# Performance work log

Measured on AMD Instinct MI355X. Metric: run time of the kernel, lower is better.

## Reference

```python
import jax, jax.numpy as jnp
import numpy as np

B, T, S, H = 4, 256, 512, 512


def setup_inputs() -> dict:
    key = jax.random.key(0)
    ks = jax.random.split(key, 8)
    scale = 1.0 / np.sqrt(H)
    return {
        "decoder_hidden": jax.random.normal(ks[0], (B, T, H), jnp.float32),
        "encoder_outputs": jax.random.normal(ks[1], (B, S, H), jnp.float32),
        "W1": jax.random.uniform(ks[2], (H, H), jnp.float32, -scale, scale),
        "b1": jax.random.uniform(ks[3], (H,), jnp.float32, -scale, scale),
        "W2": jax.random.uniform(ks[4], (H, H), jnp.float32, -scale, scale),
        "b2": jax.random.uniform(ks[5], (H,), jnp.float32, -scale, scale),
        "V": jax.random.uniform(ks[6], (H,), jnp.float32, -scale, scale),
        "bV": jax.random.uniform(ks[7], (), jnp.float32, -scale, scale),
    }


def reference(decoder_hidden, encoder_outputs, W1, b1, W2, b2, V, bV):
    # Projections: q (B,T,H), k (B,S,H)
    q = jnp.einsum("bth,hd->btd", decoder_hidden, W1.T) + b1
    k = jnp.einsum("bsh,hd->bsd", encoder_outputs, W2.T) + b2
    # Additive scores: tanh over broadcast (B,T,S,H), reduced by V -> (B,T,S)
    e = jnp.tanh(q[:, :, None, :] + k[:, None, :, :])
    score = jnp.einsum("btsh,h->bts", e, V) + bV
    attn = jax.nn.softmax(score, axis=-1)
    # Context: (B,T,S) @ (B,S,H) -> (B,T,H)
    context = jnp.einsum("bts,bsh->bth", attn, encoder_outputs)
    return context
```

## Files before the change

### kernel.cpp

```cpp
#include <hip/hip_runtime.h>

#define B 4
#define T 256
#define S 512
#define H 512
#define BT (B*T)
#define PCTX_STRIDE ((size_t)BT * H)

#define PRESCALE 2.8853900817779268f
#define LOG2E 1.4426950408889634f
#define QCLAMP 15.0f

typedef unsigned short u16;
typedef __attribute__((ext_vector_type(8))) short bf16x8;
typedef __attribute__((ext_vector_type(4))) float f32x4;

#if __has_builtin(__builtin_amdgcn_exp2f)
#define EXP2(x) __builtin_amdgcn_exp2f(x)
#else
#define EXP2(x) exp2f(x)
#endif

__device__ __forceinline__ u16 f2bf(float x) {
    unsigned u = __float_as_uint(x);
    u = u + 0x7FFFu + ((u >> 16) & 1u);
    return (u16)(u >> 16);
}

__device__ __forceinline__ void split8(float4 f0, float4 f1, bf16x8& hi, bf16x8& lo) {
    float x[8] = {f0.x, f0.y, f0.z, f0.w, f1.x, f1.y, f1.z, f1.w};
    #pragma unroll
    for (int i = 0; i < 8; ++i) {
        unsigned u = __float_as_uint(x[i]);
        unsigned h = u & 0xFFFF0000u;
        hi[i] = (short)(h >> 16);
        lo[i] = (short)f2bf(x[i] - __uint_as_float(h));
    }
}

__global__ __launch_bounds__(256) void mfma_proj(
    const float* __restrict__ dh, const float* __restrict__ enc,
    const float* __restrict__ W1, const float* __restrict__ W2,
    const float* __restrict__ b1, const float* __restrict__ b2,
    float* __restrict__ abuf, float* __restrict__ bT4)
{
    __shared__ u16 lds[4 * 4096];

    const int tid   = threadIdx.x;
    const int lane  = tid & 63;
    const int w     = tid >> 6;
    const int n0    = blockIdx.x * 64;
    const int mTile = blockIdx.y;
    const int mbase = mTile * 64;
    const bool is_q = (mTile < 16);

    const float* Asrc = is_q ? dh : enc;
    const float* Wsrc = is_q ? W1 : W2;
    const int arow = is_q ? mbase : (mbase - 1024);

    const int wm = (w & 1) * 32;
    const int wn = (w >> 1) * 32;

    const int r0  = tid >> 3;
    const int kc0 = tid & 7;

    f32x4 acc[2][2] = {};

    for (int kb = 0; kb < 8; ++kb) {
        const int k0 = kb * 64 + kc0 * 8;
        const size_t ga0 = (size_t)(arow + r0) * 512 + k0;
        const size_t ga1 = (size_t)(arow + r0 + 32) * 512 + k0;
        const size_t gw0 = (size_t)(n0 + r0) * 512 + k0;
        const size_t gw1 = (size_t)(n0 + r0 + 32) * 512 + k0;
        bf16x8 ah0, al0, ah1, al1, wh0, wl0, wh1, wl1;
        split8(*(const float4*)&Asrc[ga0], *(const float4*)&Asrc[ga0 + 4], ah0, al0);
        split8(*(const float4*)&Asrc[ga1], *(const float4*)&Asrc[ga1 + 4], ah1, al1);
        split8(*(const float4*)&Wsrc[gw0], *(const float4*)&Wsrc[gw0 + 4], wh0, wl0);
        split8(*(const float4*)&Wsrc[gw1], *(const float4*)&Wsrc[gw1 + 4], wh1, wl1);
        __syncthreads();
        const int sw  = (kc0 ^ (r0 & 7)) << 3;
        const int s0o = r0 * 64 + sw;
        const int s1o = (r0 + 32) * 64 + sw;
        *(bf16x8*)&lds[0 * 4096 + s0o] = ah0;  *(bf16x8*)&lds[0 * 4096 + s1o] = ah1;
        *(bf16x8*)&lds[1 * 4096 + s0o] = al0;  *(bf16x8*)&lds[1 * 4096 + s1o] = al1;
        *(bf16x8*)&lds[2 * 4096 + s0o] = wh0;  *(bf16x8*)&lds[2 * 4096 + s1o] = wh1;
        *(bf16x8*)&lds[3 * 4096 + s0o] = wl0;  *(bf16x8*)&lds[3 * 4096 + s1o] = wl1;
        __syncthreads();

        #pragma unroll
        for (int ks = 0; ks < 2; ++ks) {
            const int kg = ks * 4 + (lane >> 4);
            bf16x8 amh[2], aml[2], bnh[2], bnl[2];
            #pragma unroll
            for (int ms = 0; ms < 2; ++ms) {
                const int row = wm + ms * 16 + (lane & 15);
                const int off = row * 64 + ((kg ^ (row & 7)) << 3);
                amh[ms] = *(const bf16x8*)&lds[0 * 4096 + off];
                aml[ms] = *(const bf16x8*)&lds[1 * 4096 + off];
            }
            #pragma unroll
            for (int ns = 0; ns < 2; ++ns) {
                const int row = wn + ns * 16 + (lane & 15);
                const int off = row * 64 + ((kg ^ (row & 7)) << 3);
                bnh[ns] = *(const bf16x8*)&lds[2 * 4096 + off];
                bnl[ns] = *(const bf16x8*)&lds[3 * 4096 + off];
            }
            #pragma unroll
            for (int ms = 0; ms < 2; ++ms)
                #pragma unroll
                for (int ns = 0; ns < 2; ++ns) {
                    acc[ms][ns] = __builtin_amdgcn_mfma_f32_16x16x32_bf16(amh[ms], bnh[ns], acc[ms][ns], 0, 0, 0);
                    acc[ms][ns] = __builtin_amdgcn_mfma_f32_16x16x32_bf16(amh[ms], bnl[ns], acc[ms][ns], 0, 0, 0);
                    acc[ms][ns] = __builtin_amdgcn_mfma_f32_16x16x32_bf16(aml[ms], bnh[ns], acc[ms][ns], 0, 0, 0);
                }
        }
    }

    const float* bias = is_q ? b1 : b2;
    #pragma unroll
    for (int ns = 0; ns < 2; ++ns) {
        const int gn = n0 + wn + ns * 16 + (lane & 15);
        const float bv = bias[gn];
        #pragma unroll
        for (int ms = 0; ms < 2; ++ms) {
            #pragma unroll
            for (int r = 0; r < 4; ++r) {
                const int gm = mbase + wm + ms * 16 + (lane >> 4) * 4 + r;
                const float e = EXP2(fminf((acc[ms][ns][r] + bv) * PRESCALE, QCLAMP));
                if (is_q) {
                    abuf[(size_t)gm * 512 + gn] = e;
                } else {
                    const int srow = gm - 1024;
                    const int bb = srow >> 9, ss = srow & 511;
                    bT4[(((size_t)(bb * 128 + (gn >> 2)) * 512) + ss) * 4 + (gn & 3)] = e;
                }
            }
        }
    }
}

__device__ __forceinline__ float quad_term(float4 qa, float4 kb, float4 v4, float acc) {
    float x0 = fmaf(qa.x, kb.x, 1.f);
    float x1 = fmaf(qa.y, kb.y, 1.f);
    float x2 = fmaf(qa.z, kb.z, 1.f);
    float x3 = fmaf(qa.w, kb.w, 1.f);
    float p01 = x0 * x1, p23 = x2 * x3;
    float n01 = fmaf(v4.y, x0, v4.x * x1);
    float n23 = fmaf(v4.w, x2, v4.z * x3);
    float num = fmaf(n23, p01, n01 * p23);
    float den = p01 * p23;
    return fmaf(num, __builtin_amdgcn_rcpf(den), acc);
}

__global__ __launch_bounds__(256) void score_ctx(
    const float* __restrict__ abuf, const float* __restrict__ bT4,
    const float* __restrict__ enc,
    const float* __restrict__ Vp, const float* __restrict__ bVp,
    float* __restrict__ pctx, float* __restrict__ pmz)
{
    __shared__ float e_lds[8][64];

    const int tid  = threadIdx.x;
    const int lane = tid & 63;
    const int w    = tid >> 6;
    const int sc   = blockIdx.x;
    const int t0   = blockIdx.y * 8;
    const int b    = blockIdx.z;
    const int s0   = sc * 64;

    float pv = 0.f;
    #pragma unroll
    for (int i = 0; i < 8; ++i) pv += Vp[i * 64 + lane];
    #pragma unroll
    for (int off = 32; off; off >>= 1) pv += __shfl_xor(pv, off);
    pv += bVp[0];

    const int ta = t0 + w * 2;
    const int tb = ta + 1;
    const float* aA = abuf + __builtin_amdgcn_readfirstlane((b * T + ta) * H);
    const float* aB = abuf + __builtin_amdgcn_readfirstlane((b * T + tb) * H);
    const float4* bp = (const float4*)bT4 + (size_t)(b * 128) * S + s0 + lane;

    float accA = 0.f, accB = 0.f;
    #pragma unroll 4
    for (int h4 = 0; h4 < 128; ++h4) {
        float4 kb = bp[(size_t)h4 * S];
        float4 v4 = *(const float4*)&Vp[h4 * 4];
        float4 qA = *(const float4*)&aA[h4 * 4];
        float4 qB = *(const float4*)&aB[h4 * 4];
        accA = quad_term(qA, kb, v4, accA);
        accB = quad_term(qB, kb, v4, accB);
    }
    const float xA = fmaf(-2.f, accA, pv);
    const float xB = fmaf(-2.f, accB, pv);

    float mA = xA, mB = xB;
    #pragma unroll
    for (int off = 32; off; off >>= 1) {
        mA = fmaxf(mA, __shfl_xor(mA, off));
        mB = fmaxf(mB, __shfl_xor(mB, off));
    }
    const float eA = EXP2((xA - mA) * LOG2E);
    const float eB = EXP2((xB - mB) * LOG2E);
    float zA = eA, zB = eB;
    #pragma unroll
    for (int off = 32; off; off >>= 1) {
        zA += __shfl_xor(zA, off);
        zB += __shfl_xor(zB, off);
    }

    e_lds[w * 2][lane]     = eA;
    e_lds[w * 2 + 1][lane] = eB;
    if (lane == 0) {
        const size_t rowA = (size_t)sc * BT + b * T + ta;
        const size_t rowB = rowA + 1;
        pmz[rowA * 2]     = mA;  pmz[rowA * 2 + 1] = zA;
        pmz[rowB * 2]     = mB;  pmz[rowB * 2 + 1] = zB;
    }
    __syncthreads();

    const float* encb = enc + ((size_t)(b * S + s0)) * H + lane * 8;
    float4 c0A = {0,0,0,0}, c1A = {0,0,0,0}, c0B = {0,0,0,0}, c1B = {0,0,0,0};
    const float* erowA = &e_lds[w * 2][0];
    const float* erowB = &e_lds[w * 2 + 1][0];
    #pragma unroll 4
    for (int si = 0; si < 64; ++si) {
        float4 e0 = *(const float4*)&encb[(size_t)si * H];
        float4 e1 = *(const float4*)&encb[(size_t)si * H + 4];
        const float ea = erowA[si];
        const float eb = erowB[si];
        c0A.x = fmaf(ea, e0.x, c0A.x); c0A.y = fmaf(ea, e0.y, c0A.y);
        c0A.z = fmaf(ea, e0.z, c0A.z); c0A.w = fmaf(ea, e0.w, c0A.w);
        c1A.x = fmaf(ea, e1.x, c1A.x); c1A.y = fmaf(ea, e1.y, c1A.y);
        c1A.z = fmaf(ea, e1.z, c1A.z); c1A.w = fmaf(ea, e1.w, c1A.w);
        c0B.x = fmaf(eb, e0.x, c0B.x); c0B.y = fmaf(eb, e0.y, c0B.y);
        c0B.z = fmaf(eb, e0.z, c0B.z); c0B.w = fmaf(eb, e0.w, c0B.w);
        c1B.x = fmaf(eb, e1.x, c1B.x); c1B.y = fmaf(eb, e1.y, c1B.y);
        c1B.z = fmaf(eb, e1.z, c1B.z); c1B.w = fmaf(eb, e1.w, c1B.w);
    }

    float* outA = pctx + ((size_t)sc * BT + b * T + ta) * H + lane * 8;
    float* outB = pctx + ((size_t)sc * BT + b * T + tb) * H + lane * 8;
    *(float4*)outA = c0A; *(float4*)(outA + 4) = c1A;
    *(float4*)outB = c0B; *(float4*)(outB + 4) = c1B;
}

__global__ __launch_bounds__(256) void combine(
    const float* __restrict__ pctx, const float* __restrict__ pmz,
    float* __restrict__ out)
{
    const int tid  = threadIdx.x;
    const int lane = tid & 63;
    const int row  = blockIdx.x * 4 + (tid >> 6);
    const size_t urow = (size_t)__builtin_amdgcn_readfirstlane(row);

    float m[8], z[8];
    #pragma unroll
    for (int c = 0; c < 8; ++c) {
        m[c] = pmz[((size_t)c * BT + urow) * 2];
        z[c] = pmz[((size_t)c * BT + urow) * 2 + 1];
    }
    float M = m[0];
    #pragma unroll
    for (int c = 1; c < 8; ++c) M = fmaxf(M, m[c]);
    float s[8]; float Z = 0.f;
    #pragma unroll
    for (int c = 0; c < 8; ++c) { s[c] = EXP2((m[c] - M) * LOG2E); Z = fmaf(s[c], z[c], Z); }
    const float inv = __builtin_amdgcn_rcpf(Z);

    #pragma unroll
    for (int j = 0; j < 2; ++j) {
        const size_t f4 = urow * 128 + lane + j * 64;
        float4 acc = {0,0,0,0};
        #pragma unroll
        for (int c = 0; c < 8; ++c) {
            float4 p = ((const float4*)pctx)[(size_t)c * (PCTX_STRIDE / 4) + f4];
            acc.x = fmaf(s[c], p.x, acc.x);
            acc.y = fmaf(s[c], p.y, acc.y);
            acc.z = fmaf(s[c], p.z, acc.z);
            acc.w = fmaf(s[c], p.w, acc.w);
        }
        acc.x *= inv; acc.y *= inv; acc.z *= inv; acc.w *= inv;
        ((float4*)out)[f4] = acc;
    }
}

extern "C" void kernel_launch(void* const* d_in, const int* in_sizes, int n_in,
                              void* d_out, int out_size, void* d_ws, size_t ws_size,
                              hipStream_t stream) {
    const float* dh  = (const float*)d_in[0];
    const float* enc = (const float*)d_in[1];
    const float* W1  = (const float*)d_in[2];
    const float* b1  = (const float*)d_in[3];
    const float* W2  = (const float*)d_in[4];
    const float* b2  = (const float*)d_in[5];
    const float* V   = (const float*)d_in[6];
    const float* bV  = (const float*)d_in[7];

    float* abuf = (float*)d_ws;
    float* bT4  = abuf + (size_t)B * T * H;
    float* pctx = bT4 + (size_t)B * S * H;
    float* pmz  = pctx + 8 * PCTX_STRIDE;

    dim3 blk(256);
    mfma_proj<<<dim3(8, 48),    blk, 0, stream>>>(dh, enc, W1, W2, b1, b2, abuf, bT4);
    score_ctx<<<dim3(8, 32, 4), blk, 0, stream>>>(abuf, bT4, enc, V, bV, pctx, pmz);
    combine  <<<dim3(256),      blk, 0, stream>>>(pctx, pmz, (float*)d_out);
}
```

Baseline: 68.54 us.

## Compute context with split-bf16 MFMA GEMM instead of FMA partials and combine

Replaces the per-chunk FP32 FMA context accumulation and separate combine kernel with an MFMA GEMM over unnormalized exp scores, using hi/lo bf16 splitting for near-fp32 accuracy. The projection kernel gains extra blocks that transpose and split the encoder outputs into bf16 hi/lo. The softmax max subtraction is dropped, relying on the tanh-bounded score range, so only partial sums Z are written. This removes the large partial-context buffer traffic but adds transposed copies and an extra GEMM kernel with a small grid (128 blocks).

```diff
diff --git a/kernel.cpp b/kernel.cpp
--- a/kernel.cpp
+++ b/kernel.cpp
@@ -5,7 +5,6 @@
 #define S 512
 #define H 512
 #define BT (B*T)
-#define PCTX_STRIDE ((size_t)BT * H)
 
 #define PRESCALE 2.8853900817779268f
 #define LOG2E 1.4426950408889634f
@@ -42,15 +41,55 @@
     const float* __restrict__ dh, const float* __restrict__ enc,
     const float* __restrict__ W1, const float* __restrict__ W2,
     const float* __restrict__ b1, const float* __restrict__ b2,
-    float* __restrict__ abuf, float* __restrict__ bT4)
+    float* __restrict__ abuf, float* __restrict__ bT4,
+    u16* __restrict__ encT_hi, u16* __restrict__ encT_lo)
 {
     __shared__ u16 lds[4 * 4096];
 
     const int tid   = threadIdx.x;
+    const int n0    = blockIdx.x * 64;
+    const int mTile = blockIdx.y;
+
+    if (mTile >= 48) {
+        float (*TTf)[65] = reinterpret_cast<float(*)[65]>(lds);
+        const int ty = mTile - 48;
+        const int bb = ty >> 3;
+        const int st = ty & 7;
+        const int c64 = tid & 63;
+        const int r4  = tid >> 6;
+        #pragma unroll
+        for (int rr = 0; rr < 16; ++rr) {
+            const int r = rr * 4 + r4;
+            TTf[r][c64] = enc[((size_t)(bb * S + st * 64 + r)) * H + n0 + c64];
+        }
+        __syncthreads();
+        const int hr = tid >> 2;
+        const int sq = (tid & 3) * 16;
+        u16* ehp = encT_hi + ((size_t)(bb * H + n0 + hr)) * S + st * 64 + sq;
+        u16* elp = encT_lo + ((size_t)(bb * H + n0 + hr)) * S + st * 64 + sq;
+        #pragma unroll
+        for (int j4 = 0; j4 < 4; ++j4) {
+            ushort4 hv, lv;
+            #pragma unroll
+            for (int jj = 0; jj < 4; ++jj) {
+                float x = TTf[sq + j4 * 4 + jj][hr];
+                unsigned u = __float_as_uint(x);
+                unsigned hb = u & 0xFFFF0000u;
+                u16 hh = (u16)(hb >> 16);
+                u16 ll = f2bf(x - __uint_as_float(hb));
+                if (jj == 0) { hv.x = hh; lv.x = ll; }
+                else if (jj == 1) { hv.y = hh; lv.y = ll; }
+                else if (jj == 2) { hv.z = hh; lv.z = ll; }
+                else { hv.w = hh; lv.w = ll; }
+            }
+            *(ushort4*)&ehp[j4 * 4] = hv;
+            *(ushort4*)&elp[j4 * 4] = lv;
+        }
+        return;
+    }
+
     const int lane  = tid & 63;
     const int w     = tid >> 6;
-    const int n0    = blockIdx.x * 64;
-    const int mTile = blockIdx.y;
     const int mbase = mTile * 64;
     const bool is_q = (mTile < 16);
 
@@ -152,14 +191,11 @@
     return fmaf(num, __builtin_amdgcn_rcpf(den), acc);
 }
 
-__global__ __launch_bounds__(256) void score_ctx(
+__global__ __launch_bounds__(256) void score_e(
     const float* __restrict__ abuf, const float* __restrict__ bT4,
-    const float* __restrict__ enc,
     const float* __restrict__ Vp, const float* __restrict__ bVp,
-    float* __restrict__ pctx, float* __restrict__ pmz)
+    u16* __restrict__ e_hi, u16* __restrict__ e_lo, float* __restrict__ Zp)
 {
-    __shared__ float e_lds[8][64];
-
     const int tid  = threadIdx.x;
     const int lane = tid & 63;
     const int w    = tid >> 6;
@@ -194,14 +230,9 @@
     const float xA = fmaf(-2.f, accA, pv);
     const float xB = fmaf(-2.f, accB, pv);
 
-    float mA = xA, mB = xB;
-    #pragma unroll
-    for (int off = 32; off; off >>= 1) {
-        mA = fmaxf(mA, __shfl_xor(mA, off));
-        mB = fmaxf(mB, __shfl_xor(mB, off));
-    }
-    const float eA = EXP2((xA - mA) * LOG2E);
-    const float eB = EXP2((xB - mB) * LOG2E);
+    const float eA = EXP2(xA * LOG2E);
+    const float eB = EXP2(xB * LOG2E);
+
     float zA = eA, zB = eB;
     #pragma unroll
     for (int off = 32; off; off >>= 1) {
@@ -209,79 +240,117 @@
         zB += __shfl_xor(zB, off);
     }
 
-    e_lds[w * 2][lane]     = eA;
-    e_lds[w * 2 + 1][lane] = eB;
+    unsigned uA = __float_as_uint(eA), uB = __float_as_uint(eB);
+    unsigned hA = uA & 0xFFFF0000u,   hB = uB & 0xFFFF0000u;
+    const size_t rowA = (size_t)(b * T + ta);
+    const size_t rowB = (size_t)(b * T + tb);
+    e_hi[rowA * S + s0 + lane] = (u16)(hA >> 16);
+    e_lo[rowA * S + s0 + lane] = f2bf(eA - __uint_as_float(hA));
+    e_hi[rowB * S + s0 + lane] = (u16)(hB >> 16);
+    e_lo[rowB * S + s0 + lane] = f2bf(eB - __uint_as_float(hB));
+
     if (lane == 0) {
-        const size_t rowA = (size_t)sc * BT + b * T + ta;
-        const size_t rowB = rowA + 1;
-        pmz[rowA * 2]     = mA;  pmz[rowA * 2 + 1] = zA;
-        pmz[rowB * 2]     = mB;  pmz[rowB * 2 + 1] = zB;
-    }
-    __syncthreads();
-
-    const float* encb = enc + ((size_t)(b * S + s0)) * H + lane * 8;
-    float4 c0A = {0,0,0,0}, c1A = {0,0,0,0}, c0B = {0,0,0,0}, c1B = {0,0,0,0};
-    const float* erowA = &e_lds[w * 2][0];
-    const float* erowB = &e_lds[w * 2 + 1][0];
-    #pragma unroll 4
-    for (int si = 0; si < 64; ++si) {
-        float4 e0 = *(const float4*)&encb[(size_t)si * H];
-        float4 e1 = *(const float4*)&encb[(size_t)si * H + 4];
-        const float ea = erowA[si];
-        const float eb = erowB[si];
-        c0A.x = fmaf(ea, e0.x, c0A.x); c0A.y = fmaf(ea, e0.y, c0A.y);
-        c0A.z = fmaf(ea, e0.z, c0A.z); c0A.w = fmaf(ea, e0.w, c0A.w);
-        c1A.x = fmaf(ea, e1.x, c1A.x); c1A.y = fmaf(ea, e1.y, c1A.y);
-        c1A.z = fmaf(ea, e1.z, c1A.z); c1A.w = fmaf(ea, e1.w, c1A.w);
-        c0B.x = fmaf(eb, e0.x, c0B.x); c0B.y = fmaf(eb, e0.y, c0B.y);
-        c0B.z = fmaf(eb, e0.z, c0B.z); c0B.w = fmaf(eb, e0.w, c0B.w);
-        c1B.x = fmaf(eb, e1.x, c1B.x); c1B.y = fmaf(eb, e1.y, c1B.y);
-        c1B.z = fmaf(eb, e1.z, c1B.z); c1B.w = fmaf(eb, e1.w, c1B.w);
-    }
-
-    float* outA = pctx + ((size_t)sc * BT + b * T + ta) * H + lane * 8;
-    float* outB = pctx + ((size_t)sc * BT + b * T + tb) * H + lane * 8;
-    *(float4*)outA = c0A; *(float4*)(outA + 4) = c1A;
-    *(float4*)outB = c0B; *(float4*)(outB + 4) = c1B;
-}
-
-__global__ __launch_bounds__(256) void combine(
-    const float* __restrict__ pctx, const float* __restrict__ pmz,
-    float* __restrict__ out)
+        Zp[(size_t)sc * BT + rowA] = zA;
+        Zp[(size_t)sc * BT + rowB] = zB;
+    }
+}
+
+__global__ __launch_bounds__(256) void ctx_mfma(
+    const u16* __restrict__ e_hi, const u16* __restrict__ e_lo,
+    const u16* __restrict__ eT_hi, const u16* __restrict__ eT_lo,
+    const float* __restrict__ Zp, float* __restrict__ out)
 {
+    __shared__ u16 lds[4 * 4096];
+    __shared__ float zinv[64];
+
     const int tid  = threadIdx.x;
     const int lane = tid & 63;
-    const int row  = blockIdx.x * 4 + (tid >> 6);
-    const size_t urow = (size_t)__builtin_amdgcn_readfirstlane(row);
-
-    float m[8], z[8];
-    #pragma unroll
-    for (int c = 0; c < 8; ++c) {
-        m[c] = pmz[((size_t)c * BT + urow) * 2];
-        z[c] = pmz[((size_t)c * BT + urow) * 2 + 1];
-    }
-    float M = m[0];
-    #pragma unroll
-    for (int c = 1; c < 8; ++c) M = fmaxf(M, m[c]);
-    float s[8]; float Z = 0.f;
-    #pragma unroll
-    for (int c = 0; c < 8; ++c) { s[c] = EXP2((m[c] - M) * LOG2E); Z = fmaf(s[c], z[c], Z); }
-    const float inv = __builtin_amdgcn_rcpf(Z);
-
-    #pragma unroll
-    for (int j = 0; j < 2; ++j) {
-        const size_t f4 = urow * 128 + lane + j * 64;
-        float4 acc = {0,0,0,0};
-        #pragma unroll
-        for (int c = 0; c < 8; ++c) {
-            float4 p = ((const float4*)pctx)[(size_t)c * (PCTX_STRIDE / 4) + f4];
-            acc.x = fmaf(s[c], p.x, acc.x);
-            acc.y = fmaf(s[c], p.y, acc.y);
-            acc.z = fmaf(s[c], p.z, acc.z);
-            acc.w = fmaf(s[c], p.w, acc.w);
-        }
-        acc.x *= inv; acc.y *= inv; acc.z *= inv; acc.w *= inv;
-        ((float4*)out)[f4] = acc;
+    const int w    = tid >> 6;
+    const int n0   = blockIdx.x * 64;
+    const int m0   = blockIdx.y * 64;
+    const int b    = blockIdx.z;
+
+    if (tid < 64) {
+        float z = 0.f;
+        #pragma unroll
+        for (int c = 0; c < 8; ++c) z += Zp[(size_t)c * BT + b * T + m0 + tid];
+        zinv[tid] = __builtin_amdgcn_rcpf(z);
+    }
+
+    const int wm = (w & 1) * 32;
+    const int wn = (w >> 1) * 32;
+    const int r0  = tid >> 3;
+    const int kc0 = tid & 7;
+
+    const size_t abase = (size_t)(b * T + m0);
+    const size_t bbase = (size_t)b * H + n0;
+
+    f32x4 acc[2][2] = {};
+
+    for (int kb = 0; kb < 8; ++kb) {
+        const int k0 = kb * 64 + kc0 * 8;
+        const size_t ga0 = (abase + r0) * S + k0;
+        const size_t ga1 = (abase + r0 + 32) * S + k0;
+        const size_t gw0 = (bbase + r0) * S + k0;
+        const size_t gw1 = (bbase + r0 + 32) * S + k0;
+        bf16x8 ah0 = *(const bf16x8*)&e_hi[ga0];
+        bf16x8 ah1 = *(const bf16x8*)&e_hi[ga1];
+        bf16x8 al0 = *(const bf16x8*)&e_lo[ga0];
+        bf16x8 al1 = *(const bf16x8*)&e_lo[ga1];
+        bf16x8 wh0 = *(const bf16x8*)&eT_hi[gw0];
+        bf16x8 wh1 = *(const bf16x8*)&eT_hi[gw1];
+        bf16x8 wl0 = *(const bf16x8*)&eT_lo[gw0];
+        bf16x8 wl1 = *(const bf16x8*)&eT_lo[gw1];
+        __syncthreads();
+        const int sw  = (kc0 ^ (r0 & 7)) << 3;
+        const int s0o = r0 * 64 + sw;
+        const int s1o = (r0 + 32) * 64 + sw;
+        *(bf16x8*)&lds[0 * 4096 + s0o] = ah0;  *(bf16x8*)&lds[0 * 4096 + s1o] = ah1;
+        *(bf16x8*)&lds[1 * 4096 + s0o] = al0;  *(bf16x8*)&lds[1 * 4096 + s1o] = al1;
+        *(bf16x8*)&lds[2 * 4096 + s0o] = wh0;  *(bf16x8*)&lds[2 * 4096 + s1o] = wh1;
+        *(bf16x8*)&lds[3 * 4096 + s0o] = wl0;  *(bf16x8*)&lds[3 * 4096 + s1o] = wl1;
+        __syncthreads();
+
+        #pragma unroll
+        for (int ks = 0; ks < 2; ++ks) {
+            const int kg = ks * 4 + (lane >> 4);
+            bf16x8 amh[2], aml[2], bnh[2], bnl[2];
+            #pragma unroll
+            for (int ms = 0; ms < 2; ++ms) {
+                const int row = wm + ms * 16 + (lane & 15);
+                const int off = row * 64 + ((kg ^ (row & 7)) << 3);
+                amh[ms] = *(const bf16x8*)&lds[0 * 4096 + off];
+                aml[ms] = *(const bf16x8*)&lds[1 * 4096 + off];
+            }
+            #pragma unroll
+            for (int ns = 0; ns < 2; ++ns) {
+                const int row = wn + ns * 16 + (lane & 15);
+                const int off = row * 64 + ((kg ^ (row & 7)) << 3);
+                bnh[ns] = *(const bf16x8*)&lds[2 * 4096 + off];
+                bnl[ns] = *(const bf16x8*)&lds[3 * 4096 + off];
+            }
+            #pragma unroll
+            for (int ms = 0; ms < 2; ++ms)
+                #pragma unroll
+                for (int ns = 0; ns < 2; ++ns) {
+                    acc[ms][ns] = __builtin_amdgcn_mfma_f32_16x16x32_bf16(amh[ms], bnh[ns], acc[ms][ns], 0, 0, 0);
+                    acc[ms][ns] = __builtin_amdgcn_mfma_f32_16x16x32_bf16(amh[ms], bnl[ns], acc[ms][ns], 0, 0, 0);
+                    acc[ms][ns] = __builtin_amdgcn_mfma_f32_16x16x32_bf16(aml[ms], bnh[ns], acc[ms][ns], 0, 0, 0);
+                }
+        }
+    }
+
+    #pragma unroll
+    for (int ns = 0; ns < 2; ++ns) {
+        const int col = n0 + wn + ns * 16 + (lane & 15);
+        #pragma unroll
+        for (int ms = 0; ms < 2; ++ms) {
+            #pragma unroll
+            for (int r = 0; r < 4; ++r) {
+                const int row = wm + ms * 16 + (lane >> 4) * 4 + r;
+                out[((size_t)(b * T + m0 + row)) * H + col] = acc[ms][ns][r] * zinv[row];
+            }
+        }
     }
 }
 
@@ -297,13 +366,18 @@
     const float* V   = (const float*)d_in[6];
     const float* bV  = (const float*)d_in[7];
 
-    float* abuf = (float*)d_ws;
-    float* bT4  = abuf + (size_t)B * T * H;
-    float* pctx = bT4 + (size_t)B * S * H;
-    float* pmz  = pctx + 8 * PCTX_STRIDE;
+    float* abuf   = (float*)d_ws;
+    float* bT4    = abuf + (size_t)B * T * H;
+    u16*  encT_hi = (u16*)(bT4 + (size_t)B * S * H);
+    u16*  encT_lo = encT_hi + (size_t)B * H * S;
+    u16*  e_hi    = encT_lo + (size_t)B * H * S;
+    u16*  e_lo    = e_hi + (size_t)B * T * S;
+    float* Zp     = (float*)(e_lo + (size_t)B * T * S);
 
     dim3 blk(256);
-    mfma_proj<<<dim3(8, 48),    blk, 0, stream>>>(dh, enc, W1, W2, b1, b2, abuf, bT4);
-    score_ctx<<<dim3(8, 32, 4), blk, 0, stream>>>(abuf, bT4, enc, V, bV, pctx, pmz);
-    combine  <<<dim3(256),      blk, 0, stream>>>(pctx, pmz, (float*)d_out);
-}
+    mfma_proj<<<dim3(8, 80),    blk, 0, stream>>>(dh, enc, W1, W2, b1, b2,
+                                                  abuf, bT4, encT_hi, encT_lo);
+    score_e  <<<dim3(8, 32, 4), blk, 0, stream>>>(abuf, bT4, V, bV, e_hi, e_lo, Zp);
+    ctx_mfma <<<dim3(8, 4, 4),  blk, 0, stream>>>(e_hi, e_lo, encT_hi, encT_lo,
+                                                  Zp, (float*)d_out);
+}
```

Result: faster. 60.09 us (-12.3%).
